# Kernel optimization log

Hardware: AMD Instinct MI355X
Metric: run time of the kernel (lower is better)

## Reference

```python
import jax, jax.numpy as jnp
import numpy as np

B, N, M12, H, O, I, DIFF = 8192, 100, 12, 64, 128, 12, 1.0
TWO_PI = 2.0 * np.pi


def _moments_single(xi, K):
    # xi: [N, 2] single sample; K: [12, 2] exponent pairs -> [12]
    xc = xi - xi.mean(axis=0)                 # center per-sample (mean over points)
    p = xc[:, None, :] ** K[None, :, :]       # [N, 12, 2]
    return jnp.sum(p[..., 0] * p[..., 1], axis=0)  # [12]


def setup_inputs() -> dict:
    key = jax.random.key(0)
    ks = jax.random.split(key, 8)
    # 12 integer central-moment exponent pairs (p, q)
    P = jnp.array([1, 2, 0, 2, 1, 3, 0, 2, 3, 1, 4, 0], jnp.float32)
    Q = jnp.array([1, 0, 2, 1, 2, 0, 3, 2, 1, 3, 0, 4], jnp.float32)
    K = jnp.stack([P, Q], axis=-1)            # [12, 2]

    x = jax.random.normal(ks[0], (B, N, 2), jnp.float32)
    t = jax.random.uniform(ks[1], (1,), jnp.float32, 0.1, 1.0)  # positive time
    W_fourier = jax.random.normal(ks[2], (H // 2,), jnp.float32) * 30.0

    def lin(k, fin, fout):
        bound = 1.0 / np.sqrt(fin)
        kw, kb = jax.random.split(k)
        W = jax.random.uniform(kw, (fin, fout), jnp.float32, -bound, bound)
        b = jax.random.uniform(kb, (fout,), jnp.float32, -bound, bound)
        return W, b

    embed_W, embed_b = lin(ks[3], H, H)
    lin1_W, lin1_b = lin(ks[4], I, H)
    lin2a_W, lin2a_b = lin(ks[5], H, O)
    lin2b_W, lin2b_b = lin(ks[6], O, I)
    lin2c_W, lin2c_b = lin(ks[7], I, I)
    return {
        'x': x, 't': t, 'K': K, 'W_fourier': W_fourier,
        'embed_W': embed_W, 'embed_b': embed_b,
        'lin1_W': lin1_W, 'lin1_b': lin1_b,
        'lin2a_W': lin2a_W, 'lin2a_b': lin2a_b,
        'lin2b_W': lin2b_W, 'lin2b_b': lin2b_b,
        'lin2c_W': lin2c_W, 'lin2c_b': lin2c_b,
    }


def reference(x, t, K, W_fourier, embed_W, embed_b, lin1_W, lin1_b,
              lin2a_W, lin2a_b, lin2b_W, lin2b_b, lin2c_W, lin2c_b):
    # Invariance encoding ('Moment' mode): [B, 12]
    m = jax.vmap(_moments_single, in_axes=(0, None))(x, K)
    h = jax.nn.gelu(m @ lin1_W + lin1_b, approximate=False)   # [B, H] (dropout = eval identity)
    # Gaussian Fourier time embedding: [1, H]
    xp = t[:, None] * W_fourier[None, :] * TWO_PI
    emb = jnp.concatenate([jnp.sin(xp), jnp.cos(xp)], axis=-1) @ embed_W + embed_b
    h = jax.nn.gelu((h + emb) @ lin2a_W + lin2a_b, approximate=False)
    h = jax.nn.gelu(h @ lin2b_W + lin2b_b, approximate=False)
    h = (h @ lin2c_W + lin2c_b) / jnp.sqrt(DIFF * t)          # [B, 12]
    # Per-sample jacobian of the moment map: [B, 12, N, 2]
    # (equals the block diagonal of torch.autograd.functional.jacobian over the batch)
    jac = jax.vmap(jax.jacrev(_moments_single), in_axes=(0, None))(x, K)
    # Replaces the (i, j) double loop of tiny matmuls with one batched contraction
    return jnp.einsum('bk,bknj->bnj', h, jac)                 # [B, N, 2]
```

## Files before the change

kernel.cpp:

```cpp
#include <hip/hip_runtime.h>


static __device__ __forceinline__ float gelu_f(float x) {
    float y = 0.7071067811865475f * x;
    float s = fabsf(y);
    float t = __builtin_amdgcn_rcpf(fmaf(0.3275911f, s, 1.0f));
    float p = t * fmaf(t, fmaf(t, fmaf(t, fmaf(t, 1.061405429f,
                    -1.453152027f), 1.421413741f), -0.284496736f), 0.254829592f);
    float e = __expf(-y * y);
    float ea = fmaf(-p, e, 1.0f);
    float erfv = copysignf(ea, y);
    return 0.5f * x * (1.0f + erfv);
}

#define DPP_ADD(v, ctrl) \
    v += __int_as_float(__builtin_amdgcn_update_dpp(0, __float_as_int(v), ctrl, 0xf, 0xf, true))

static __device__ __forceinline__ float wave_sum(float v) {
    DPP_ADD(v, 0x111);
    DPP_ADD(v, 0x112);
    DPP_ADD(v, 0x114);
    DPP_ADD(v, 0x118);
    DPP_ADD(v, 0x142);
    DPP_ADD(v, 0x143);
    return __int_as_float(__builtin_amdgcn_readlane(__float_as_int(v), 63));
}

#define TWO_PI_F 6.283185307179586f

__global__ __launch_bounds__(256) void scorenet_fused(
    const float* __restrict__ x,
    const float* __restrict__ t_in,
    const float* __restrict__ Wf,
    const float* __restrict__ embW,
    const float* __restrict__ embB,
    const float* __restrict__ W1,
    const float* __restrict__ b1,
    const float* __restrict__ W2a,
    const float* __restrict__ b2a,
    const float* __restrict__ W2b,
    const float* __restrict__ b2b,
    const float* __restrict__ W2c,
    const float* __restrict__ b2c,
    float* __restrict__ out,
    int B)
{
    __shared__ float s_f[64];
    __shared__ float s_epart[4][64];
    __shared__ float s_a[64][4];
    __shared__ float s_part[4][2][4][64];
    __shared__ float s_w2bT[12][128];

    const int tid = threadIdx.x;
    const int lane = tid & 63;
    const int w = tid >> 6;
    const float tval = t_in[0];

    const int sb0 = blockIdx.x * 8 + w;
    const int sb1 = sb0 + 4;
    const bool v0 = sb0 < B, v1 = sb1 < B;
    const int c0i = v0 ? sb0 : B - 1;
    const int c1i = v1 ? sb1 : B - 1;

    const bool has2 = lane < 36;
    const float2* px0 = reinterpret_cast<const float2*>(x) + (size_t)c0i * 100;
    const float2* px1 = reinterpret_cast<const float2*>(x) + (size_t)c1i * 100;
    float2 pA[2], pB[2];
    pA[0] = px0[lane];  pB[0] = px0[has2 ? lane + 64 : lane];
    pA[1] = px1[lane];  pB[1] = px1[has2 ? lane + 64 : lane];

    #pragma unroll
    for (int i = tid; i < 1536; i += 256) {
        int row = i / 12, col = i - row * 12;
        s_w2bT[col][row] = W2b[i];
    }

    if (tid < 32) {
        float xp = tval * Wf[tid] * TWO_PI_F;
        s_f[tid]      = sinf(xp);
        s_f[tid + 32] = cosf(xp);
    }
    __syncthreads();

    {
        float ep = 0.0f;
        #pragma unroll
        for (int jj = 0; jj < 16; ++jj) {
            int j = 16 * w + jj;
            ep = fmaf(s_f[j], embW[j * 64 + lane], ep);
        }
        s_epart[w][lane] = ep;
    }
    __syncthreads();

    const float embl = embB[lane]
        + ((s_epart[0][lane] + s_epart[1][lane])
         + (s_epart[2][lane] + s_epart[3][lane]));
    const float rst = rsqrtf(tval);

    const float2* w2a2 = reinterpret_cast<const float2*>(W2a);
    const float2 bb2a = reinterpret_cast<const float2*>(b2a)[lane];

    #pragma unroll
    for (int g = 0; g < 2; ++g) {
        const bool valid = g ? v1 : v0;
        const int bc = g ? c1i : c0i;

        float xa = pA[g].x, ya = pA[g].y;
        float xb = has2 ? pB[g].x : 0.0f;
        float yb = has2 ? pB[g].y : 0.0f;

        const float mux = wave_sum(xa + xb) * 0.01f;
        const float muy = wave_sum(ya + yb) * 0.01f;

        float ua = xa - mux, va = ya - muy;
        float ub = has2 ? (xb - mux) : 0.0f;
        float vb = has2 ? (yb - muy) : 0.0f;

        float ms[12];
        {
            float u2 = ua * ua, v2 = va * va;
            ms[0] = ua * va;   ms[1] = u2;        ms[2] = v2;
            ms[3] = u2 * va;   ms[4] = ua * v2;
            ms[5] = u2 * ua;   ms[6] = v2 * va;
            ms[7] = u2 * v2;   ms[8] = ms[5] * va; ms[9] = ua * ms[6];
            ms[10] = u2 * u2;  ms[11] = v2 * v2;
            float w2 = ub * ub, z2 = vb * vb;
            ms[0] += ub * vb;  ms[1] += w2;       ms[2] += z2;
            ms[3] += w2 * vb;  ms[4] += ub * z2;
            ms[5] += w2 * ub;  ms[6] += z2 * vb;
            ms[7] += w2 * z2;  ms[8] += w2 * ub * vb; ms[9] += ub * z2 * vb;
            ms[10] += w2 * w2; ms[11] += z2 * z2;
        }
        float m[12];
        #pragma unroll
        for (int k = 0; k < 12; ++k) m[k] = wave_sum(ms[k]);

        float a1 = b1[lane];
        #pragma unroll
        for (int k = 0; k < 12; ++k) a1 = fmaf(m[k], W1[k * 64 + lane], a1);
        float aval = gelu_f(a1) + embl;

        s_a[lane][w] = aval;
        __syncthreads();

        float4 plo = {0.f, 0.f, 0.f, 0.f};
        float4 phi = {0.f, 0.f, 0.f, 0.f};
        {
            const float4* a4p = reinterpret_cast<const float4*>(&s_a[0][0]);
            #pragma unroll
            for (int jj = 0; jj < 16; ++jj) {
                const int j = (w << 4) + jj;
                float4 a4 = a4p[j];
                float2 ww = w2a2[j * 64 + lane];
                plo.x = fmaf(a4.x, ww.x, plo.x);
                plo.y = fmaf(a4.y, ww.x, plo.y);
                plo.z = fmaf(a4.z, ww.x, plo.z);
                plo.w = fmaf(a4.w, ww.x, plo.w);
                phi.x = fmaf(a4.x, ww.y, phi.x);
                phi.y = fmaf(a4.y, ww.y, phi.y);
                phi.z = fmaf(a4.z, ww.y, phi.z);
                phi.w = fmaf(a4.w, ww.y, phi.w);
            }
        }
        s_part[0][0][w][lane] = plo.x;
        s_part[1][0][w][lane] = plo.y;
        s_part[2][0][w][lane] = plo.z;
        s_part[3][0][w][lane] = plo.w;
        s_part[0][1][w][lane] = phi.x;
        s_part[1][1][w][lane] = phi.y;
        s_part[2][1][w][lane] = phi.z;
        s_part[3][1][w][lane] = phi.w;
        __syncthreads();

        float acc0 = bb2a.x + ((s_part[w][0][0][lane] + s_part[w][0][1][lane])
                             + (s_part[w][0][2][lane] + s_part[w][0][3][lane]));
        float acc1 = bb2a.y + ((s_part[w][1][0][lane] + s_part[w][1][1][lane])
                             + (s_part[w][1][2][lane] + s_part[w][1][3][lane]));
        float h2lo = gelu_f(acc0), h2hi = gelu_f(acc1);

        float h3[12];
        #pragma unroll
        for (int k = 0; k < 12; ++k) {
            float2 wk = *reinterpret_cast<const float2*>(&s_w2bT[k][2 * lane]);
            float p3 = fmaf(h2lo, wk.x, h2hi * wk.y);
            h3[k] = gelu_f(wave_sum(p3) + b2b[k]);
        }

        float hk = 0.0f;
        if (lane < 12) {
            hk = b2c[lane];
            #pragma unroll
            for (int j = 0; j < 12; ++j) hk = fmaf(h3[j], W2c[j * 12 + lane], hk);
            hk *= rst;
        }
        float h[12];
        #pragma unroll
        for (int k = 0; k < 12; ++k)
            h[k] = __int_as_float(__builtin_amdgcn_readlane(__float_as_int(hk), k));

        const float inv_n = 0.01f;
        float cc0 = (2.0f*h[3]*m[0] + h[4]*m[2] + 3.0f*h[5]*m[1] + 2.0f*h[7]*m[4]
                   + 3.0f*h[8]*m[3] + h[9]*m[6] + 4.0f*h[10]*m[5]) * inv_n;
        float cc1 = (h[3]*m[1] + 2.0f*h[4]*m[0] + 3.0f*h[6]*m[2] + 2.0f*h[7]*m[3]
                   + h[8]*m[5] + 3.0f*h[9]*m[4] + 4.0f*h[11]*m[6]) * inv_n;

        const float A1 = 2.0f*h[1], A2 = h[0],      A3 = 3.0f*h[5], A4 = 2.0f*h[3], A5 = h[4];
        const float A6 = 4.0f*h[10],A7 = 3.0f*h[8], A8 = 2.0f*h[7], A9 = h[9];
        const float B1 = h[0],      B2 = 2.0f*h[2], B3 = h[3],      B4 = 2.0f*h[4], B5 = 3.0f*h[6];
        const float B6 = h[8],      B7 = 2.0f*h[7], B8 = 3.0f*h[9], B9 = 4.0f*h[11];

        float2* pout = reinterpret_cast<float2*>(out) + (size_t)bc * 100;
        if (valid) {
            float u = ua, v = va;
            float u2 = u*u, v2 = v*v;
            float o0 = A1*u + A2*v + A3*u2 + A4*u*v + A5*v2 + A6*u2*u + A7*u2*v + A8*u*v2 + A9*v2*v - cc0;
            float o1 = B1*u + B2*v + B3*u2 + B4*u*v + B5*v2 + B6*u2*u + B7*u2*v + B8*u*v2 + B9*v2*v - cc1;
            float2 r; r.x = o0; r.y = o1;
            pout[lane] = r;
            if (has2) {
                float uu = ub, vv = vb;
                float uu2 = uu*uu, vv2 = vv*vv;
                float q0 = A1*uu + A2*vv + A3*uu2 + A4*uu*vv + A5*vv2 + A6*uu2*uu + A7*uu2*vv + A8*uu*vv2 + A9*vv2*vv - cc0;
                float q1 = B1*uu + B2*vv + B3*uu2 + B4*uu*vv + B5*vv2 + B6*uu2*uu + B7*uu2*vv + B8*uu*vv2 + B9*vv2*vv - cc1;
                float2 r2; r2.x = q0; r2.y = q1;
                pout[lane + 64] = r2;
            }
        }
    }
}

extern "C" void kernel_launch(void* const* d_in, const int* in_sizes, int n_in,
                              void* d_out, int out_size, void* d_ws, size_t ws_size,
                              hipStream_t stream) {
    const float* x    = (const float*)d_in[0];
    const float* t    = (const float*)d_in[1];
    const float* Wf   = (const float*)d_in[3];
    const float* embW = (const float*)d_in[4];
    const float* embB = (const float*)d_in[5];
    const float* W1   = (const float*)d_in[6];
    const float* b1   = (const float*)d_in[7];
    const float* W2a  = (const float*)d_in[8];
    const float* b2a  = (const float*)d_in[9];
    const float* W2b  = (const float*)d_in[10];
    const float* b2b  = (const float*)d_in[11];
    const float* W2c  = (const float*)d_in[12];
    const float* b2c  = (const float*)d_in[13];

    const int B = in_sizes[0] / 200;
    const int blocks = (B + 7) / 8;

    scorenet_fused<<<blocks, 256, 0, stream>>>(
        x, t, Wf, embW, embB, W1, b1, W2a, b2a, W2b, b2b, W2c, b2c,
        (float*)d_out, B);
}
```

Measured before the change: 95.99 us.

## Batch both sample groups through shared-memory stages to cut block barriers

The kernel now computes the moments for both sample groups up front. It runs the lin1 and lin2a stages for both groups together, using double-buffered shared arrays, so the per-group barriers inside the loop collapse into fewer block-wide syncs. The W2a slice is preloaded into registers before the loop, and the Fourier sin/cos values are kept in registers and broadcast with readlane instead of going through shared memory. This raises register pressure and shared memory use, and it adds a launch-bounds occupancy hint that may force spills.

```diff
diff --git a/kernel.cpp b/kernel.cpp
--- a/kernel.cpp
+++ b/kernel.cpp
@@ -28,7 +28,7 @@
 
 #define TWO_PI_F 6.283185307179586f
 
-__global__ __launch_bounds__(256) void scorenet_fused(
+__global__ __launch_bounds__(256, 4) void scorenet_fused(
     const float* __restrict__ x,
     const float* __restrict__ t_in,
     const float* __restrict__ Wf,
@@ -45,10 +45,9 @@
     float* __restrict__ out,
     int B)
 {
-    __shared__ float s_f[64];
     __shared__ float s_epart[4][64];
-    __shared__ float s_a[64][4];
-    __shared__ float s_part[4][2][4][64];
+    __shared__ float s_a[2][64][4];
+    __shared__ float s_part[2][4][2][4][64];
     __shared__ float s_w2bT[12][128];
 
     const int tid = threadIdx.x;
@@ -69,28 +68,69 @@
     pA[0] = px0[lane];  pB[0] = px0[has2 ? lane + 64 : lane];
     pA[1] = px1[lane];  pB[1] = px1[has2 ? lane + 64 : lane];
 
+    float2 wreg[16];
+    {
+        const float2* w2a2 = reinterpret_cast<const float2*>(W2a);
+        #pragma unroll
+        for (int jj = 0; jj < 16; ++jj)
+            wreg[jj] = w2a2[((w << 4) + jj) * 64 + lane];
+    }
+
     #pragma unroll
     for (int i = tid; i < 1536; i += 256) {
         int row = i / 12, col = i - row * 12;
         s_w2bT[col][row] = W2b[i];
     }
 
-    if (tid < 32) {
-        float xp = tval * Wf[tid] * TWO_PI_F;
-        s_f[tid]      = sinf(xp);
-        s_f[tid + 32] = cosf(xp);
-    }
-    __syncthreads();
+    float fxp = tval * Wf[lane & 31] * TWO_PI_F;
+    float f = (lane < 32) ? sinf(fxp) : cosf(fxp);
 
     {
         float ep = 0.0f;
         #pragma unroll
         for (int jj = 0; jj < 16; ++jj) {
-            int j = 16 * w + jj;
-            ep = fmaf(s_f[j], embW[j * 64 + lane], ep);
+            int j = (w << 4) + jj;
+            float fj = __int_as_float(__builtin_amdgcn_readlane(__float_as_int(f), j));
+            ep = fmaf(fj, embW[j * 64 + lane], ep);
         }
         s_epart[w][lane] = ep;
     }
+
+    float ua[2], va[2], ub[2], vb[2];
+    float m[2][12];
+    #pragma unroll
+    for (int g = 0; g < 2; ++g) {
+        float xa = pA[g].x, ya = pA[g].y;
+        float xb = has2 ? pB[g].x : 0.0f;
+        float yb = has2 ? pB[g].y : 0.0f;
+
+        const float mux = wave_sum(xa + xb) * 0.01f;
+        const float muy = wave_sum(ya + yb) * 0.01f;
+
+        ua[g] = xa - mux;  va[g] = ya - muy;
+        ub[g] = has2 ? (xb - mux) : 0.0f;
+        vb[g] = has2 ? (yb - muy) : 0.0f;
+
+        float ms[12];
+        {
+            float uA = ua[g], vA = va[g], uB = ub[g], vB = vb[g];
+            float u2 = uA * uA, v2 = vA * vA;
+            ms[0] = uA * vA;   ms[1] = u2;        ms[2] = v2;
+            ms[3] = u2 * vA;   ms[4] = uA * v2;
+            ms[5] = u2 * uA;   ms[6] = v2 * vA;
+            ms[7] = u2 * v2;   ms[8] = ms[5] * vA; ms[9] = uA * ms[6];
+            ms[10] = u2 * u2;  ms[11] = v2 * v2;
+            float w2 = uB * uB, z2 = vB * vB;
+            ms[0] += uB * vB;  ms[1] += w2;       ms[2] += z2;
+            ms[3] += w2 * vB;  ms[4] += uB * z2;
+            ms[5] += w2 * uB;  ms[6] += z2 * vB;
+            ms[7] += w2 * z2;  ms[8] += w2 * uB * vB; ms[9] += uB * z2 * vB;
+            ms[10] += w2 * w2; ms[11] += z2 * z2;
+        }
+        #pragma unroll
+        for (int k = 0; k < 12; ++k) m[g][k] = wave_sum(ms[k]);
+    }
+
     __syncthreads();
 
     const float embl = embB[lane]
@@ -98,7 +138,48 @@
          + (s_epart[2][lane] + s_epart[3][lane]));
     const float rst = rsqrtf(tval);
 
-    const float2* w2a2 = reinterpret_cast<const float2*>(W2a);
+    {
+        float a10 = b1[lane], a11 = b1[lane];
+        #pragma unroll
+        for (int k = 0; k < 12; ++k) {
+            float wk = W1[k * 64 + lane];
+            a10 = fmaf(m[0][k], wk, a10);
+            a11 = fmaf(m[1][k], wk, a11);
+        }
+        s_a[0][lane][w] = gelu_f(a10) + embl;
+        s_a[1][lane][w] = gelu_f(a11) + embl;
+    }
+    __syncthreads();
+
+    #pragma unroll
+    for (int g = 0; g < 2; ++g) {
+        float4 plo = {0.f, 0.f, 0.f, 0.f};
+        float4 phi = {0.f, 0.f, 0.f, 0.f};
+        const float4* a4p = reinterpret_cast<const float4*>(&s_a[g][0][0]);
+        #pragma unroll
+        for (int jj = 0; jj < 16; ++jj) {
+            float4 a4 = a4p[(w << 4) + jj];
+            float2 ww = wreg[jj];
+            plo.x = fmaf(a4.x, ww.x, plo.x);
+            plo.y = fmaf(a4.y, ww.x, plo.y);
+            plo.z = fmaf(a4.z, ww.x, plo.z);
+            plo.w = fmaf(a4.w, ww.x, plo.w);
+            phi.x = fmaf(a4.x, ww.y, phi.x);
+            phi.y = fmaf(a4.y, ww.y, phi.y);
+            phi.z = fmaf(a4.z, ww.y, phi.z);
+            phi.w = fmaf(a4.w, ww.y, phi.w);
+        }
+        s_part[g][0][0][w][lane] = plo.x;
+        s_part[g][1][0][w][lane] = plo.y;
+        s_part[g][2][0][w][lane] = plo.z;
+        s_part[g][3][0][w][lane] = plo.w;
+        s_part[g][0][1][w][lane] = phi.x;
+        s_part[g][1][1][w][lane] = phi.y;
+        s_part[g][2][1][w][lane] = phi.z;
+        s_part[g][3][1][w][lane] = phi.w;
+    }
+    __syncthreads();
+
     const float2 bb2a = reinterpret_cast<const float2*>(b2a)[lane];
 
     #pragma unroll
@@ -106,77 +187,10 @@
         const bool valid = g ? v1 : v0;
         const int bc = g ? c1i : c0i;
 
-        float xa = pA[g].x, ya = pA[g].y;
-        float xb = has2 ? pB[g].x : 0.0f;
-        float yb = has2 ? pB[g].y : 0.0f;
-
-        const float mux = wave_sum(xa + xb) * 0.01f;
-        const float muy = wave_sum(ya + yb) * 0.01f;
-
-        float ua = xa - mux, va = ya - muy;
-        float ub = has2 ? (xb - mux) : 0.0f;
-        float vb = has2 ? (yb - muy) : 0.0f;
-
-        float ms[12];
-        {
-            float u2 = ua * ua, v2 = va * va;
-            ms[0] = ua * va;   ms[1] = u2;        ms[2] = v2;
-            ms[3] = u2 * va;   ms[4] = ua * v2;
-            ms[5] = u2 * ua;   ms[6] = v2 * va;
-            ms[7] = u2 * v2;   ms[8] = ms[5] * va; ms[9] = ua * ms[6];
-            ms[10] = u2 * u2;  ms[11] = v2 * v2;
-            float w2 = ub * ub, z2 = vb * vb;
-            ms[0] += ub * vb;  ms[1] += w2;       ms[2] += z2;
-            ms[3] += w2 * vb;  ms[4] += ub * z2;
-            ms[5] += w2 * ub;  ms[6] += z2 * vb;
-            ms[7] += w2 * z2;  ms[8] += w2 * ub * vb; ms[9] += ub * z2 * vb;
-            ms[10] += w2 * w2; ms[11] += z2 * z2;
-        }
-        float m[12];
-        #pragma unroll
-        for (int k = 0; k < 12; ++k) m[k] = wave_sum(ms[k]);
-
-        float a1 = b1[lane];
-        #pragma unroll
-        for (int k = 0; k < 12; ++k) a1 = fmaf(m[k], W1[k * 64 + lane], a1);
-        float aval = gelu_f(a1) + embl;
-
-        s_a[lane][w] = aval;
-        __syncthreads();
-
-        float4 plo = {0.f, 0.f, 0.f, 0.f};
-        float4 phi = {0.f, 0.f, 0.f, 0.f};
-        {
-            const float4* a4p = reinterpret_cast<const float4*>(&s_a[0][0]);
-            #pragma unroll
-            for (int jj = 0; jj < 16; ++jj) {
-                const int j = (w << 4) + jj;
-                float4 a4 = a4p[j];
-                float2 ww = w2a2[j * 64 + lane];
-                plo.x = fmaf(a4.x, ww.x, plo.x);
-                plo.y = fmaf(a4.y, ww.x, plo.y);
-                plo.z = fmaf(a4.z, ww.x, plo.z);
-                plo.w = fmaf(a4.w, ww.x, plo.w);
-                phi.x = fmaf(a4.x, ww.y, phi.x);
-                phi.y = fmaf(a4.y, ww.y, phi.y);
-                phi.z = fmaf(a4.z, ww.y, phi.z);
-                phi.w = fmaf(a4.w, ww.y, phi.w);
-            }
-        }
-        s_part[0][0][w][lane] = plo.x;
-        s_part[1][0][w][lane] = plo.y;
-        s_part[2][0][w][lane] = plo.z;
-        s_part[3][0][w][lane] = plo.w;
-        s_part[0][1][w][lane] = phi.x;
-        s_part[1][1][w][lane] = phi.y;
-        s_part[2][1][w][lane] = phi.z;
-        s_part[3][1][w][lane] = phi.w;
-        __syncthreads();
-
-        float acc0 = bb2a.x + ((s_part[w][0][0][lane] + s_part[w][0][1][lane])
-                             + (s_part[w][0][2][lane] + s_part[w][0][3][lane]));
-        float acc1 = bb2a.y + ((s_part[w][1][0][lane] + s_part[w][1][1][lane])
-                             + (s_part[w][1][2][lane] + s_part[w][1][3][lane]));
+        float acc0 = bb2a.x + ((s_part[g][w][0][0][lane] + s_part[g][w][0][1][lane])
+                             + (s_part[g][w][0][2][lane] + s_part[g][w][0][3][lane]));
+        float acc1 = bb2a.y + ((s_part[g][w][1][0][lane] + s_part[g][w][1][1][lane])
+                             + (s_part[g][w][1][2][lane] + s_part[g][w][1][3][lane]));
         float h2lo = gelu_f(acc0), h2hi = gelu_f(acc1);
 
         float h3[12];
@@ -200,10 +214,10 @@
             h[k] = __int_as_float(__builtin_amdgcn_readlane(__float_as_int(hk), k));
 
         const float inv_n = 0.01f;
-        float cc0 = (2.0f*h[3]*m[0] + h[4]*m[2] + 3.0f*h[5]*m[1] + 2.0f*h[7]*m[4]
-                   + 3.0f*h[8]*m[3] + h[9]*m[6] + 4.0f*h[10]*m[5]) * inv_n;
-        float cc1 = (h[3]*m[1] + 2.0f*h[4]*m[0] + 3.0f*h[6]*m[2] + 2.0f*h[7]*m[3]
-                   + h[8]*m[5] + 3.0f*h[9]*m[4] + 4.0f*h[11]*m[6]) * inv_n;
+        float cc0 = (2.0f*h[3]*m[g][0] + h[4]*m[g][2] + 3.0f*h[5]*m[g][1] + 2.0f*h[7]*m[g][4]
+                   + 3.0f*h[8]*m[g][3] + h[9]*m[g][6] + 4.0f*h[10]*m[g][5]) * inv_n;
+        float cc1 = (h[3]*m[g][1] + 2.0f*h[4]*m[g][0] + 3.0f*h[6]*m[g][2] + 2.0f*h[7]*m[g][3]
+                   + h[8]*m[g][5] + 3.0f*h[9]*m[g][4] + 4.0f*h[11]*m[g][6]) * inv_n;
 
         const float A1 = 2.0f*h[1], A2 = h[0],      A3 = 3.0f*h[5], A4 = 2.0f*h[3], A5 = h[4];
         const float A6 = 4.0f*h[10],A7 = 3.0f*h[8], A8 = 2.0f*h[7], A9 = h[9];
@@ -212,14 +226,14 @@
 
         float2* pout = reinterpret_cast<float2*>(out) + (size_t)bc * 100;
         if (valid) {
-            float u = ua, v = va;
+            float u = ua[g], v = va[g];
             float u2 = u*u, v2 = v*v;
             float o0 = A1*u + A2*v + A3*u2 + A4*u*v + A5*v2 + A6*u2*u + A7*u2*v + A8*u*v2 + A9*v2*v - cc0;
             float o1 = B1*u + B2*v + B3*u2 + B4*u*v + B5*v2 + B6*u2*u + B7*u2*v + B8*u*v2 + B9*v2*v - cc1;
             float2 r; r.x = o0; r.y = o1;
             pout[lane] = r;
             if (has2) {
-                float uu = ub, vv = vb;
+                float uu = ub[g], vv = vb[g];
                 float uu2 = uu*uu, vv2 = vv*vv;
                 float q0 = A1*uu + A2*vv + A3*uu2 + A4*uu*vv + A5*vv2 + A6*uu2*uu + A7*uu2*vv + A8*uu*vv2 + A9*vv2*vv - cc0;
                 float q1 = B1*uu + B2*vv + B3*uu2 + B4*uu*vv + B5*vv2 + B6*uu2*uu + B7*uu2*vv + B8*uu*vv2 + B9*vv2*vv - cc1;
```

New measurement: 97.68 us. Within noise of the previous version (+1.8%).
